# Performance work log

Hardware: AMD Instinct MI355X
Metric: run time of the kernel (lower is better)

## Reference

```python
import jax, jax.numpy as jnp
import numpy as np

N_HEADS, D_MODEL, DK, DV = 16, 1024, 64, 64
B, S = 4, 2048
NEG = -1000000000.0


def setup_inputs() -> dict:
    key = jax.random.key(0)
    ks = jax.random.split(key, 10)
    inp = {
        "q": jax.random.normal(ks[0], (B, S, D_MODEL), jnp.float32),
        "k": jax.random.normal(ks[1], (B, S, D_MODEL), jnp.float32),
        "v": jax.random.normal(ks[2], (B, S, D_MODEL), jnp.float32),
        "padding_mask": jax.random.randint(ks[3], (B, 1, S), 0, 2, jnp.int32),
        # linear params (torch Linear: y = x @ W.T + b); store as [in, out]
        "w_q": jax.random.normal(ks[4], (D_MODEL, N_HEADS * DK), jnp.float32) * 0.02,
        "b_q": jnp.zeros((N_HEADS * DK,), jnp.float32),
        "w_k": jax.random.normal(ks[5], (D_MODEL, N_HEADS * DK), jnp.float32) * 0.02,
        "b_k": jnp.zeros((N_HEADS * DK,), jnp.float32),
        "w_v": jax.random.normal(ks[6], (D_MODEL, N_HEADS * DV), jnp.float32) * 0.02,
        "b_v": jnp.zeros((N_HEADS * DV,), jnp.float32),
    }
    return inp


def reference(q, k, v, padding_mask, w_q, b_q, w_k, b_k, w_v, b_v):
    residual = q
    # project and split heads: [B, H, S, dk]
    qh = (q @ w_q + b_q).reshape(B, S, N_HEADS, DK).transpose(0, 2, 1, 3)
    kh = (k @ w_k + b_k).reshape(B, S, N_HEADS, DK).transpose(0, 2, 1, 3)
    vh = (v @ w_v + b_v).reshape(B, S, N_HEADS, DV).transpose(0, 2, 1, 3)
    # NB: original code DIVIDES by factor = dk**-0.5, i.e. multiplies by sqrt(dk)
    scores = jnp.einsum("bhqd,bhkd->bhqk", qh, kh) / (DK ** -0.5)
    mask = padding_mask[:, None, :, :]  # [B,1,1,S] broadcasts over heads/queries
    scores = jnp.where(mask == 0, NEG, scores)
    attn = jax.nn.softmax(scores, axis=-1)  # dropout = identity (eval)
    ctx = jnp.einsum("bhqk,bhkd->bhqd", attn, vh)
    ctx = ctx.transpose(0, 2, 1, 3).reshape(B, S, N_HEADS * DV)
    return ctx + residual
```

## Files before the change

kernel.cpp:

```cpp
#include <hip/hip_runtime.h>
#include <hip/hip_fp16.h>

#define BB 4
#define SS 2048
#define HH 16
#define DKK 64
#define DMODEL 1024

typedef __attribute__((ext_vector_type(8))) _Float16 half8;
typedef __attribute__((ext_vector_type(2))) __fp16 fp16x2;
typedef __attribute__((ext_vector_type(4))) float floatx4;

#define MFMA16(a, b, c) __builtin_amdgcn_mfma_f32_16x16x32_f16(a, b, c, 0, 0, 0)

#define SCL2 11.5415603336f

__device__ __forceinline__ void gload_lds16(const _Float16* g, _Float16* l) {
    __builtin_amdgcn_global_load_lds(
        (const __attribute__((address_space(1))) void*)g,
        (__attribute__((address_space(3))) void*)l, 16, 0, 0);
}

__device__ __forceinline__
void convert_x_body(const float* __restrict__ src, _Float16* __restrict__ dst,
                    int bidx)
{
    size_t base = ((size_t)bidx * 256 + threadIdx.x) * 8;
    int m = (int)(base >> 10);
    int kk = (int)(base & 1023);
    float4 a = *(const float4*)(src + base);
    float4 b = *(const float4*)(src + base + 4);
    half8 h;
    h[0] = (_Float16)a.x; h[1] = (_Float16)a.y; h[2] = (_Float16)a.z; h[3] = (_Float16)a.w;
    h[4] = (_Float16)b.x; h[5] = (_Float16)b.y; h[6] = (_Float16)b.z; h[7] = (_Float16)b.w;
    int kd = kk ^ ((m & 7) << 3);
    *(half8*)(dst + ((size_t)m << 10) + kd) = h;
}

__device__ __forceinline__
void convert_wt_body(const float* __restrict__ W, _Float16* __restrict__ WT,
                     int bidx)
{
    __shared__ __attribute__((aligned(16))) _Float16 T[64][72];
    int kt = (bidx >> 4) << 6;
    int nt = (bidx & 15) << 6;
    int tid = threadIdx.x;
    #pragma unroll
    for (int p = 0; p < 4; p++) {
        int lin = tid + p * 256;
        int row = lin >> 4;
        int c4 = (lin & 15) << 2;
        float4 vv = *(const float4*)(W + (size_t)(kt + row) * DMODEL + nt + c4);
        T[c4 + 0][row] = (_Float16)vv.x;
        T[c4 + 1][row] = (_Float16)vv.y;
        T[c4 + 2][row] = (_Float16)vv.z;
        T[c4 + 3][row] = (_Float16)vv.w;
    }
    __syncthreads();
    #pragma unroll
    for (int p = 0; p < 2; p++) {
        int lin = tid + p * 256;
        int nl = lin >> 3;
        int u = lin & 7;
        half8 h = *(const half8*)&T[nl][u * 8];
        int n = nt + nl;
        int kd = kt + ((u ^ (n & 7)) << 3);
        *(half8*)(WT + (size_t)n * DMODEL + kd) = h;
    }
}

__global__ __launch_bounds__(256)
void convert_x(const float* __restrict__ q, const float* __restrict__ k,
               const float* __restrict__ v, _Float16* __restrict__ xq,
               _Float16* __restrict__ xk, _Float16* __restrict__ xv)
{
    int z = blockIdx.y;
    convert_x_body(z == 0 ? q : z == 1 ? k : v,
                   z == 0 ? xq : z == 1 ? xk : xv, blockIdx.x);
}

__global__ __launch_bounds__(256)
void convert_wt(const float* __restrict__ wq, const float* __restrict__ wk,
                const float* __restrict__ wv, _Float16* __restrict__ tq,
                _Float16* __restrict__ tk, _Float16* __restrict__ tv)
{
    int z = blockIdx.y;
    convert_wt_body(z == 0 ? wq : z == 1 ? wk : wv,
                    z == 0 ? tq : z == 1 ? tk : tv, blockIdx.x);
}

__global__ __launch_bounds__(256)
void convert_all(const float* __restrict__ q, const float* __restrict__ k,
                 const float* __restrict__ v, const float* __restrict__ wq,
                 const float* __restrict__ wk, const float* __restrict__ wv,
                 _Float16* __restrict__ xq, _Float16* __restrict__ xk,
                 _Float16* __restrict__ xv, _Float16* __restrict__ tq,
                 _Float16* __restrict__ tk, _Float16* __restrict__ tv)
{
    int y = blockIdx.y;
    if (y < 3) {
        convert_x_body(y == 0 ? q : y == 1 ? k : v,
                       y == 0 ? xq : y == 1 ? xk : xv, blockIdx.x);
    } else {
        if (blockIdx.x >= 768) return;
        int z = blockIdx.x >> 8;
        convert_wt_body(z == 0 ? wq : z == 1 ? wk : wv,
                        z == 0 ? tq : z == 1 ? tk : tv, blockIdx.x & 255);
    }
}

template <int VMODE>
__device__ __forceinline__
void proj_body(const _Float16* __restrict__ X, const _Float16* __restrict__ WT,
               const float* __restrict__ bias, _Float16* __restrict__ out,
               int bidx)
{
    __shared__ __attribute__((aligned(16))) _Float16 As[128 * 64];
    __shared__ __attribute__((aligned(16))) _Float16 Bs[128 * 64];
    const int tid = threadIdx.x;
    const int wave = tid >> 6, lane = tid & 63, quad = lane >> 4, l16 = lane & 15;
    const int wm = wave >> 1, wn = wave & 1;
    const int m0 = ((bidx & 7) | ((bidx >> 6) << 3)) << 7;
    const int n0 = ((bidx >> 3) & 7) << 7;
    const int lrow = lane >> 3;
    const int lcol = (lane & 7) << 3;

    floatx4 acc[4][4] = {};

    for (int k0 = 0; k0 < DMODEL; k0 += 64) {
        __syncthreads();
        #pragma unroll
        for (int c = 0; c < 4; c++) {
            int row = c * 32 + wave * 8;
            gload_lds16(X + (size_t)(m0 + row + lrow) * DMODEL + k0 + lcol,
                        As + (size_t)row * 64);
            gload_lds16(WT + (size_t)(n0 + row + lrow) * DMODEL + k0 + lcol,
                        Bs + (size_t)row * 64);
        }
        __syncthreads();
        #pragma unroll
        for (int ks = 0; ks < 2; ks++) {
            int ccol = ((ks * 4 + quad) ^ (l16 & 7)) << 3;
            half8 af[4], bf[4];
            #pragma unroll
            for (int i = 0; i < 4; i++)
                af[i] = *(const half8*)(As + (wm * 64 + i * 16 + l16) * 64 + ccol);
            #pragma unroll
            for (int j = 0; j < 4; j++)
                bf[j] = *(const half8*)(Bs + (wn * 64 + j * 16 + l16) * 64 + ccol);
            #pragma unroll
            for (int i = 0; i < 4; i++)
                #pragma unroll
                for (int j = 0; j < 4; j++)
                    acc[i][j] = VMODE ? MFMA16(bf[j], af[i], acc[i][j])
                                      : MFMA16(af[i], bf[j], acc[i][j]);
        }
    }

    if (VMODE == 0) {
        #pragma unroll
        for (int j = 0; j < 4; j++) {
            int ng = n0 + wn * 64 + j * 16 + l16;
            int h = ng >> 6, d = ng & 63;
            float bv = bias[ng];
            #pragma unroll
            for (int i = 0; i < 4; i++)
                #pragma unroll
                for (int r = 0; r < 4; r++) {
                    int mg = m0 + wm * 64 + i * 16 + quad * 4 + r;
                    int bb = mg >> 11, s = mg & 2047;
                    out[(((size_t)bb * HH + h) * SS + s) * DKK + d] =
                        (_Float16)(acc[i][j][r] + bv);
                }
        }
    } else {
        #pragma unroll
        for (int j = 0; j < 4; j++)
            #pragma unroll
            for (int r = 0; r < 4; r++) {
                int ng = n0 + wn * 64 + j * 16 + quad * 4 + r;
                int h = ng >> 6, d = ng & 63;
                float bv = bias[ng];
                #pragma unroll
                for (int i = 0; i < 4; i++) {
                    int mg = m0 + wm * 64 + i * 16 + l16;
                    int bb = mg >> 11, s = mg & 2047;
                    out[(((size_t)bb * HH + h) * DKK + d) * SS + s] =
                        (_Float16)(acc[i][j][r] + bv);
                }
            }
    }
}

template <int VMODE>
__global__ __launch_bounds__(256)
void proj128(const _Float16* __restrict__ X, const _Float16* __restrict__ WT,
             const float* __restrict__ bias, _Float16* __restrict__ out)
{
    proj_body<VMODE>(X, WT, bias, out, blockIdx.x);
}

__global__ __launch_bounds__(256)
void proj_all(const _Float16* __restrict__ Xq, const _Float16* __restrict__ Xk,
              const _Float16* __restrict__ Xv, const _Float16* __restrict__ WTq,
              const _Float16* __restrict__ WTk, const _Float16* __restrict__ WTv,
              const float* __restrict__ bq, const float* __restrict__ bk,
              const float* __restrict__ bv, _Float16* __restrict__ Qh,
              _Float16* __restrict__ Kh, _Float16* __restrict__ VTh)
{
    int z = blockIdx.y;
    if (z == 0)      proj_body<0>(Xq, WTq, bq, Qh, blockIdx.x);
    else if (z == 1) proj_body<0>(Xk, WTk, bk, Kh, blockIdx.x);
    else             proj_body<1>(Xv, WTv, bv, VTh, blockIdx.x);
}

__global__ __launch_bounds__(256)
void flash3(const _Float16* __restrict__ Qw, const _Float16* __restrict__ Kw,
            const _Float16* __restrict__ VTw, const int* __restrict__ mask,
            const float* __restrict__ resid, float* __restrict__ out)
{
    __shared__ float Bias[SS];
    __shared__ __attribute__((aligned(16))) _Float16 Plds[4][2][16][72];

    const int tid = threadIdx.x;
    const int wave = tid >> 6, lane = tid & 63, quad = lane >> 4, l16 = lane & 15;
    const int bx = blockIdx.x;
    const int xcd = bx & 7;
    const int jj = bx >> 3;
    const int bh = ((jj >> 4) << 3) | xcd;
    const int qt = jj & 15;
    const int b = bh >> 4;
    const int h = bh & 15;
    const int qbase = qt * 128 + wave * 32;

    const int* mk = mask + b * SS;
    for (int i = tid; i < SS; i += 256)
        Bias[i] = mk[i] ? 0.f : -1.0e9f;
    __syncthreads();

    half8 qf[2][2];
    #pragma unroll
    for (int mt = 0; mt < 2; mt++) {
        const _Float16* Qp = Qw + ((size_t)bh * SS + qbase + mt * 16 + l16) * DKK;
        qf[mt][0] = *(const half8*)(Qp + quad * 8);
        qf[mt][1] = *(const half8*)(Qp + 32 + quad * 8);
    }

    float mrow[2] = {-3.0e38f, -3.0e38f};
    float lrow[2] = {0.f, 0.f};
    floatx4 oacc[2][4] = {};

    const _Float16* Kbase = Kw + (size_t)bh * SS * DKK;
    const _Float16* Vbase = VTw + (size_t)bh * DKK * SS;

    for (int kt = 0; kt < SS / 64; kt++) {
        const int kb = kt * 64;

        half8 kf[2][4];
        #pragma unroll
        for (int ks = 0; ks < 2; ks++)
            #pragma unroll
            for (int k2 = 0; k2 < 4; k2++)
                kf[ks][k2] = *(const half8*)(Kbase
                    + (size_t)(kb + k2 * 16 + l16) * DKK + ks * 32 + quad * 8);

        floatx4 sacc[2][4] = {};
        #pragma unroll
        for (int mt = 0; mt < 2; mt++)
            #pragma unroll
            for (int ks = 0; ks < 2; ks++)
                #pragma unroll
                for (int k2 = 0; k2 < 4; k2++)
                    sacc[mt][k2] = MFMA16(kf[ks][k2], qf[mt][ks], sacc[mt][k2]);

        half8 vf[2][4];
        #pragma unroll
        for (int ks = 0; ks < 2; ks++)
            #pragma unroll
            for (int dt = 0; dt < 4; dt++)
                vf[ks][dt] = *(const half8*)(Vbase
                    + (size_t)(dt * 16 + l16) * SS + kb + ks * 32 + quad * 8);

        float4 bs[4];
        #pragma unroll
        for (int k2 = 0; k2 < 4; k2++)
            bs[k2] = *(const float4*)&Bias[kb + k2 * 16 + quad * 4];

        #pragma unroll
        for (int mt = 0; mt < 2; mt++) {
            float p[4][4];
            #pragma unroll
            for (int k2 = 0; k2 < 4; k2++) {
                const float* bp = (const float*)&bs[k2];
                #pragma unroll
                for (int r = 0; r < 4; r++)
                    p[k2][r] = fmaf(sacc[mt][k2][r], SCL2, bp[r]);
            }
            float t = p[0][0];
            #pragma unroll
            for (int k2 = 0; k2 < 4; k2++)
                #pragma unroll
                for (int r = 0; r < 4; r++)
                    t = fmaxf(t, p[k2][r]);
            t = fmaxf(t, __shfl_xor(t, 16, 64));
            t = fmaxf(t, __shfl_xor(t, 32, 64));
            float mn = fmaxf(mrow[mt], t);
            float al = exp2f(mrow[mt] - mn);
            mrow[mt] = mn;

            float ps = 0.f;
            #pragma unroll
            for (int k2 = 0; k2 < 4; k2++)
                #pragma unroll
                for (int r = 0; r < 4; r++) {
                    float pv = exp2f(p[k2][r] - mn);
                    p[k2][r] = pv;
                    ps += pv;
                }
            ps += __shfl_xor(ps, 16, 64);
            ps += __shfl_xor(ps, 32, 64);
            lrow[mt] = lrow[mt] * al + ps;

            #pragma unroll
            for (int k2 = 0; k2 < 4; k2++) {
                fp16x2 pa = __builtin_amdgcn_cvt_pkrtz(p[k2][0], p[k2][1]);
                fp16x2 pb = __builtin_amdgcn_cvt_pkrtz(p[k2][2], p[k2][3]);
                *(fp16x2*)&Plds[wave][mt][l16][k2 * 16 + quad * 4]     = pa;
                *(fp16x2*)&Plds[wave][mt][l16][k2 * 16 + quad * 4 + 2] = pb;
            }
            #pragma unroll
            for (int dt = 0; dt < 4; dt++)
                oacc[mt][dt] *= al;

            #pragma unroll
            for (int ks = 0; ks < 2; ks++) {
                half8 pf = *(const half8*)&Plds[wave][mt][l16][ks * 32 + quad * 8];
                #pragma unroll
                for (int dt = 0; dt < 4; dt++)
                    oacc[mt][dt] = MFMA16(vf[ks][dt], pf, oacc[mt][dt]);
            }
        }
    }

    #pragma unroll
    for (int mt = 0; mt < 2; mt++) {
        float rl = 1.0f / lrow[mt];
        int s = qbase + mt * 16 + l16;
        size_t rowoff = ((size_t)b * SS + s) * DMODEL + h * DKK;
        #pragma unroll
        for (int dt = 0; dt < 4; dt++) {
            size_t gi = rowoff + dt * 16 + quad * 4;
            float4 rv = *(const float4*)&resid[gi];
            float4 ov;
            ov.x = oacc[mt][dt][0] * rl + rv.x;
            ov.y = oacc[mt][dt][1] * rl + rv.y;
            ov.z = oacc[mt][dt][2] * rl + rv.z;
            ov.w = oacc[mt][dt][3] * rl + rv.w;
            *(float4*)&out[gi] = ov;
        }
    }
}

extern "C" void kernel_launch(void* const* d_in, const int* in_sizes, int n_in,
                              void* d_out, int out_size, void* d_ws, size_t ws_size,
                              hipStream_t stream)
{
    const float* q    = (const float*)d_in[0];
    const float* k    = (const float*)d_in[1];
    const float* v    = (const float*)d_in[2];
    const int*   mask = (const int*)d_in[3];
    const float* wq   = (const float*)d_in[4];
    const float* bq   = (const float*)d_in[5];
    const float* wk   = (const float*)d_in[6];
    const float* bk   = (const float*)d_in[7];
    const float* wv   = (const float*)d_in[8];
    const float* bv   = (const float*)d_in[9];
    float* out = (float*)d_out;

    const size_t TENS = (size_t)BB * SS * HH * DKK;
    const size_t WSZ  = (size_t)DMODEL * DMODEL;
    _Float16* base = (_Float16*)d_ws;

    bool big = ws_size >= (6 * TENS + 3 * WSZ) * sizeof(_Float16);
    _Float16 *Xq, *Xk, *Xv, *Qh, *Kh, *VTh, *WTq;
    if (big) {
        Xq = base;            Xk = base + TENS;     Xv = base + 2 * TENS;
        Qh = base + 3 * TENS; Kh = base + 4 * TENS; VTh = base + 5 * TENS;
        WTq = base + 6 * TENS;
    } else {
        Xq = base;            Xk = base + TENS;     Xv = base + 2 * TENS;
        Qh = base + 3 * TENS; Kh = Xq;              VTh = Xk;
        WTq = base + 4 * TENS;
    }
    _Float16* WTk = WTq + WSZ;
    _Float16* WTv = WTk + WSZ;

    if (big) {
        hipLaunchKernelGGL(convert_all, dim3(4096, 4), dim3(256), 0, stream,
                           q, k, v, wq, wk, wv, Xq, Xk, Xv, WTq, WTk, WTv);
        hipLaunchKernelGGL(proj_all, dim3(512, 3), dim3(256), 0, stream,
                           Xq, Xk, Xv, WTq, WTk, WTv, bq, bk, bv, Qh, Kh, VTh);
    } else {
        hipLaunchKernelGGL(convert_x, dim3(4096, 3), dim3(256), 0, stream,
                           q, k, v, Xq, Xk, Xv);
        hipLaunchKernelGGL(convert_wt, dim3(256, 3), dim3(256), 0, stream,
                           wq, wk, wv, WTq, WTk, WTv);
        hipLaunchKernelGGL((proj128<0>), dim3(512), dim3(256), 0, stream, Xq, WTq, bq, Qh);
        hipLaunchKernelGGL((proj128<0>), dim3(512), dim3(256), 0, stream, Xk, WTk, bk, Kh);
        hipLaunchKernelGGL((proj128<1>), dim3(512), dim3(256), 0, stream, Xv, WTv, bv, VTh);
    }
    hipLaunchKernelGGL(flash3, dim3(BB * HH * (SS / 128)), dim3(256), 0, stream,
                       Qh, Kh, VTh, mask, q, out);
}
```

Before: 456.2 us.

## Fold score scale into Q projection, seed scores with mask bias, lazy rescale, swizzle P LDS

Multiplies Q by the softmax scale (times log2e) in the projection epilogue, so the attention kernel no longer does a per-score FMA. Score accumulators are initialised with the mask bias so MFMA adds it directly. The running max and rescale of the output accumulator are skipped when no row's max increases (wave ballot). The padded P staging buffer becomes an XOR-swizzled unpadded layout written with 64-bit stores, and launch bounds request 3 blocks per CU. Scaling Q before the fp16 rounding changes Q's magnitude in fp16 and may affect precision.

```diff
diff --git a/kernel.cpp b/kernel.cpp
--- a/kernel.cpp
+++ b/kernel.cpp
@@ -8,6 +8,7 @@
 #define DMODEL 1024
 
 typedef __attribute__((ext_vector_type(8))) _Float16 half8;
+typedef __attribute__((ext_vector_type(4))) _Float16 half4;
 typedef __attribute__((ext_vector_type(2))) __fp16 fp16x2;
 typedef __attribute__((ext_vector_type(4))) float floatx4;
 
@@ -113,7 +114,7 @@
 __device__ __forceinline__
 void proj_body(const _Float16* __restrict__ X, const _Float16* __restrict__ WT,
                const float* __restrict__ bias, _Float16* __restrict__ out,
-               int bidx)
+               int bidx, float scl)
 {
     __shared__ __attribute__((aligned(16))) _Float16 As[128 * 64];
     __shared__ __attribute__((aligned(16))) _Float16 Bs[128 * 64];
@@ -170,7 +171,7 @@
                     int mg = m0 + wm * 64 + i * 16 + quad * 4 + r;
                     int bb = mg >> 11, s = mg & 2047;
                     out[(((size_t)bb * HH + h) * SS + s) * DKK + d] =
-                        (_Float16)(acc[i][j][r] + bv);
+                        (_Float16)((acc[i][j][r] + bv) * scl);
                 }
         }
     } else {
@@ -186,7 +187,7 @@
                     int mg = m0 + wm * 64 + i * 16 + l16;
                     int bb = mg >> 11, s = mg & 2047;
                     out[(((size_t)bb * HH + h) * DKK + d) * SS + s] =
-                        (_Float16)(acc[i][j][r] + bv);
+                        (_Float16)((acc[i][j][r] + bv) * scl);
                 }
             }
     }
@@ -195,9 +196,9 @@
 template <int VMODE>
 __global__ __launch_bounds__(256)
 void proj128(const _Float16* __restrict__ X, const _Float16* __restrict__ WT,
-             const float* __restrict__ bias, _Float16* __restrict__ out)
-{
-    proj_body<VMODE>(X, WT, bias, out, blockIdx.x);
+             const float* __restrict__ bias, _Float16* __restrict__ out, float scl)
+{
+    proj_body<VMODE>(X, WT, bias, out, blockIdx.x, scl);
 }
 
 __global__ __launch_bounds__(256)
@@ -209,18 +210,18 @@
               _Float16* __restrict__ Kh, _Float16* __restrict__ VTh)
 {
     int z = blockIdx.y;
-    if (z == 0)      proj_body<0>(Xq, WTq, bq, Qh, blockIdx.x);
-    else if (z == 1) proj_body<0>(Xk, WTk, bk, Kh, blockIdx.x);
-    else             proj_body<1>(Xv, WTv, bv, VTh, blockIdx.x);
-}
-
-__global__ __launch_bounds__(256)
+    if (z == 0)      proj_body<0>(Xq, WTq, bq, Qh, blockIdx.x, SCL2);
+    else if (z == 1) proj_body<0>(Xk, WTk, bk, Kh, blockIdx.x, 1.0f);
+    else             proj_body<1>(Xv, WTv, bv, VTh, blockIdx.x, 1.0f);
+}
+
+__global__ __launch_bounds__(256, 3)
 void flash3(const _Float16* __restrict__ Qw, const _Float16* __restrict__ Kw,
             const _Float16* __restrict__ VTw, const int* __restrict__ mask,
             const float* __restrict__ resid, float* __restrict__ out)
 {
     __shared__ float Bias[SS];
-    __shared__ __attribute__((aligned(16))) _Float16 Plds[4][2][16][72];
+    __shared__ __attribute__((aligned(16))) _Float16 Plds[4][2][16][64];
 
     const int tid = threadIdx.x;
     const int wave = tid >> 6, lane = tid & 63, quad = lane >> 4, l16 = lane & 15;
@@ -232,6 +233,7 @@
     const int b = bh >> 4;
     const int h = bh & 15;
     const int qbase = qt * 128 + wave * 32;
+    const int sw = l16 & 7;
 
     const int* mk = mask + b * SS;
     for (int i = tid; i < SS; i += 256)
@@ -256,6 +258,15 @@
     for (int kt = 0; kt < SS / 64; kt++) {
         const int kb = kt * 64;
 
+        floatx4 sacc[2][4];
+        #pragma unroll
+        for (int k2 = 0; k2 < 4; k2++) {
+            float4 bv = *(const float4*)&Bias[kb + k2 * 16 + quad * 4];
+            floatx4 bi = {bv.x, bv.y, bv.z, bv.w};
+            sacc[0][k2] = bi;
+            sacc[1][k2] = bi;
+        }
+
         half8 kf[2][4];
         #pragma unroll
         for (int ks = 0; ks < 2; ks++)
@@ -264,7 +275,6 @@
                 kf[ks][k2] = *(const half8*)(Kbase
                     + (size_t)(kb + k2 * 16 + l16) * DKK + ks * 32 + quad * 8);
 
-        floatx4 sacc[2][4] = {};
         #pragma unroll
         for (int mt = 0; mt < 2; mt++)
             #pragma unroll
@@ -281,60 +291,56 @@
                 vf[ks][dt] = *(const half8*)(Vbase
                     + (size_t)(dt * 16 + l16) * SS + kb + ks * 32 + quad * 8);
 
-        float4 bs[4];
-        #pragma unroll
-        for (int k2 = 0; k2 < 4; k2++)
-            bs[k2] = *(const float4*)&Bias[kb + k2 * 16 + quad * 4];
-
         #pragma unroll
         for (int mt = 0; mt < 2; mt++) {
-            float p[4][4];
-            #pragma unroll
-            for (int k2 = 0; k2 < 4; k2++) {
-                const float* bp = (const float*)&bs[k2];
-                #pragma unroll
-                for (int r = 0; r < 4; r++)
-                    p[k2][r] = fmaf(sacc[mt][k2][r], SCL2, bp[r]);
-            }
-            float t = p[0][0];
+            floatx4* S = sacc[mt];
+
+            float t4[4];
             #pragma unroll
             for (int k2 = 0; k2 < 4; k2++)
-                #pragma unroll
-                for (int r = 0; r < 4; r++)
-                    t = fmaxf(t, p[k2][r]);
+                t4[k2] = fmaxf(fmaxf(S[k2][0], S[k2][1]),
+                               fmaxf(S[k2][2], S[k2][3]));
+            float t = fmaxf(fmaxf(t4[0], t4[1]), fmaxf(t4[2], t4[3]));
             t = fmaxf(t, __shfl_xor(t, 16, 64));
             t = fmaxf(t, __shfl_xor(t, 32, 64));
-            float mn = fmaxf(mrow[mt], t);
-            float al = exp2f(mrow[mt] - mn);
-            mrow[mt] = mn;
-
-            float ps = 0.f;
-            #pragma unroll
-            for (int k2 = 0; k2 < 4; k2++)
-                #pragma unroll
-                for (int r = 0; r < 4; r++) {
-                    float pv = exp2f(p[k2][r] - mn);
-                    p[k2][r] = pv;
-                    ps += pv;
-                }
+
+            if (__ballot(t > mrow[mt])) {
+                float mn = fmaxf(mrow[mt], t);
+                float al = exp2f(mrow[mt] - mn);
+                mrow[mt] = mn;
+                lrow[mt] *= al;
+                #pragma unroll
+                for (int dt = 0; dt < 4; dt++)
+                    oacc[mt][dt] *= al;
+            }
+            const float mn = mrow[mt];
+
+            float ss[4];
+            #pragma unroll
+            for (int k2 = 0; k2 < 4; k2++) {
+                #pragma unroll
+                for (int r = 0; r < 4; r++)
+                    S[k2][r] = exp2f(S[k2][r] - mn);
+                ss[k2] = (S[k2][0] + S[k2][1]) + (S[k2][2] + S[k2][3]);
+            }
+            float ps = (ss[0] + ss[1]) + (ss[2] + ss[3]);
             ps += __shfl_xor(ps, 16, 64);
             ps += __shfl_xor(ps, 32, 64);
-            lrow[mt] = lrow[mt] * al + ps;
+            lrow[mt] += ps;
 
             #pragma unroll
             for (int k2 = 0; k2 < 4; k2++) {
-                fp16x2 pa = __builtin_amdgcn_cvt_pkrtz(p[k2][0], p[k2][1]);
-                fp16x2 pb = __builtin_amdgcn_cvt_pkrtz(p[k2][2], p[k2][3]);
-                *(fp16x2*)&Plds[wave][mt][l16][k2 * 16 + quad * 4]     = pa;
-                *(fp16x2*)&Plds[wave][mt][l16][k2 * 16 + quad * 4 + 2] = pb;
+                union { fp16x2 h2[2]; half4 h4; } u;
+                u.h2[0] = __builtin_amdgcn_cvt_pkrtz(S[k2][0], S[k2][1]);
+                u.h2[1] = __builtin_amdgcn_cvt_pkrtz(S[k2][2], S[k2][3]);
+                int cbw = ((((k2 << 1) | (quad >> 1)) ^ sw) << 3) | ((quad & 1) << 2);
+                *(half4*)&Plds[wave][mt][l16][cbw] = u.h4;
             }
-            #pragma unroll
-            for (int dt = 0; dt < 4; dt++)
-                oacc[mt][dt] *= al;
 
             #pragma unroll
             for (int ks = 0; ks < 2; ks++) {
-                half8 pf = *(const half8*)&Plds[wave][mt][l16][ks * 32 + quad * 8];
+                half8 pf = *(const half8*)
+                    &Plds[wave][mt][l16][((ks * 4 + quad) ^ sw) << 3];
                 #pragma unroll
                 for (int dt = 0; dt < 4; dt++)
                     oacc[mt][dt] = MFMA16(vf[ks][dt], pf, oacc[mt][dt]);
@@ -405,9 +411,9 @@
                            q, k, v, Xq, Xk, Xv);
         hipLaunchKernelGGL(convert_wt, dim3(256, 3), dim3(256), 0, stream,
                            wq, wk, wv, WTq, WTk, WTv);
-        hipLaunchKernelGGL((proj128<0>), dim3(512), dim3(256), 0, stream, Xq, WTq, bq, Qh);
-        hipLaunchKernelGGL((proj128<0>), dim3(512), dim3(256), 0, stream, Xk, WTk, bk, Kh);
-        hipLaunchKernelGGL((proj128<1>), dim3(512), dim3(256), 0, stream, Xv, WTv, bv, VTh);
+        hipLaunchKernelGGL((proj128<0>), dim3(512), dim3(256), 0, stream, Xq, WTq, bq, Qh, SCL2);
+        hipLaunchKernelGGL((proj128<0>), dim3(512), dim3(256), 0, stream, Xk, WTk, bk, Kh, 1.0f);
+        hipLaunchKernelGGL((proj128<1>), dim3(512), dim3(256), 0, stream, Xv, WTv, bv, VTh, 1.0f);
     }
     hipLaunchKernelGGL(flash3, dim3(BB * HH * (SS / 128)), dim3(256), 0, stream,
                        Qh, Kh, VTh, mask, q, out);
```

Measured after the change: 510.1 us. 1.12x slower.
